# Kernel tuning notes

Measured on AMD Instinct MI355X. Metric: run time of the kernel, lower is better.

Reference implementation:

```python
import jax, jax.numpy as jnp
import numpy as np

DIM = 768
N_HEADS = 12
HEAD_DIM = DIM // N_HEADS
B, S = 2, 4096


def setup_inputs() -> dict:
    key = jax.random.key(0)
    k_x, k_wqkv, k_bqkv, k_wout, k_bout = jax.random.split(key, 5)
    scale_in = 1.0 / np.sqrt(DIM)
    return {
        "x": jax.random.normal(k_x, (B, S, DIM), dtype=jnp.float32),
        "Wqkv": jax.random.normal(k_wqkv, (DIM, 3 * DIM), dtype=jnp.float32) * scale_in,
        "bqkv": jax.random.normal(k_bqkv, (3 * DIM,), dtype=jnp.float32) * 0.02,
        "Wout": jax.random.normal(k_wout, (DIM, DIM), dtype=jnp.float32) * scale_in,
        "bout": jax.random.normal(k_bout, (DIM,), dtype=jnp.float32) * 0.02,
    }


def reference(x, Wqkv, bqkv, Wout, bout):
    b, s, d = x.shape
    qkv = (x @ Wqkv + bqkv).reshape(b, s, 3, N_HEADS, HEAD_DIM)
    qkv = jnp.transpose(qkv, (2, 0, 3, 1, 4))  # [3, B, H, S, hd]
    q, k, v = qkv[0], qkv[1], qkv[2]
    scale = HEAD_DIM ** -0.5
    attn = jnp.einsum('bhqd,bhkd->bhqk', q, k) * scale  # [B, H, S, S]
    causal_mask = jnp.triu(jnp.ones((s, s), dtype=bool), k=1)
    attn = jnp.where(causal_mask[None, None], -jnp.inf, attn)
    attn = jax.nn.softmax(attn, axis=-1)
    out = jnp.einsum('bhqk,bhkd->bhqd', attn, v)  # [B, H, S, hd]
    out = jnp.transpose(out, (0, 2, 1, 3)).reshape(b, s, d)
    return out @ Wout + bout
```

## Files before the change

### kernel.cpp

```cpp
#include <hip/hip_runtime.h>
#include <hip/hip_bf16.h>
#include <math.h>

#define DIM 768
#define NH 12
#define HD 64
#define BATCH 2
#define SEQ 4096
#define MTOT (BATCH * SEQ)

#define QSCALE 0.1803368801111244f

typedef unsigned short u16;
typedef __bf16 bf16x8 __attribute__((ext_vector_type(8)));
typedef float  f32x4  __attribute__((ext_vector_type(4)));
typedef float  f32x16 __attribute__((ext_vector_type(16)));
typedef unsigned short u16x4 __attribute__((ext_vector_type(4)));
typedef unsigned short u16x8 __attribute__((ext_vector_type(8)));
typedef unsigned u32x4 __attribute__((ext_vector_type(4)));

__device__ inline u16 f2bf(float f) {
    unsigned u = __builtin_bit_cast(unsigned, f);
    u += 0x7fffu + ((u >> 16) & 1u);
    return (u16)(u >> 16);
}

#if defined(__has_builtin) && __has_builtin(__builtin_amdgcn_cvt_pk_bf16_f32)
#define HAVE_PK_BF16 1
__device__ inline unsigned pk2bf(float a, float b) {
    auto v = __builtin_amdgcn_cvt_pk_bf16_f32(a, b);
    return __builtin_bit_cast(unsigned, v);
}
#else
#define HAVE_PK_BF16 0
__device__ inline unsigned pk2bf(float a, float b) {
    return (unsigned)f2bf(a) | ((unsigned)f2bf(b) << 16);
}
#endif

__device__ inline f32x4 mfma16(bf16x8 a, bf16x8 b, f32x4 c) {
    return __builtin_amdgcn_mfma_f32_16x16x32_bf16(a, b, c, 0, 0, 0);
}
__device__ inline f32x16 mfma32(bf16x8 a, bf16x8 b, f32x16 c) {
    return __builtin_amdgcn_mfma_f32_32x32x16_bf16(a, b, c, 0, 0, 0);
}

__device__ inline void gl2lds16(const u16* g, u16* l) {
    __builtin_amdgcn_global_load_lds(
        (const __attribute__((address_space(1))) void*)g,
        (__attribute__((address_space(3))) void*)l,
        16, 0, 0);
}

__global__ __launch_bounds__(256)
void cvt_bf16(const float* __restrict__ src, u16* __restrict__ dst, int n8)
{
    int i = blockIdx.x * 256 + threadIdx.x;
    if (i >= n8) return;
    float4 a = ((const float4*)src)[i * 2];
    float4 b = ((const float4*)src)[i * 2 + 1];
    u16x8 o;
    o[0] = f2bf(a.x); o[1] = f2bf(a.y); o[2] = f2bf(a.z); o[3] = f2bf(a.w);
    o[4] = f2bf(b.x); o[5] = f2bf(b.y); o[6] = f2bf(b.z); o[7] = f2bf(b.w);
    ((u16x8*)dst)[i] = o;
}

__global__ __launch_bounds__(256)
void transpose_to_bf16(const float* __restrict__ src, u16* __restrict__ dst,
                       int R, int C)
{
    __shared__ float tile[32][33];
    const int c0 = blockIdx.x * 32, r0 = blockIdx.y * 32;
    const int tx = threadIdx.x & 31, ty = threadIdx.x >> 5;
#pragma unroll
    for (int i = 0; i < 4; ++i) {
        int row = ty * 4 + i;
        tile[row][tx] = src[(size_t)(r0 + row) * C + c0 + tx];
    }
    __syncthreads();
#pragma unroll
    for (int i = 0; i < 4; ++i) {
        int crow = ty * 4 + i;
        dst[(size_t)(c0 + crow) * R + r0 + tx] = f2bf(tile[tx][crow]);
    }
}

__device__ inline void gemm_lds_mainloop(const u16* __restrict__ Ag,
                                         const u16* __restrict__ Bg,
                                         int m0, int n0, int w, int lane,
                                         u16 (*As)[64 * 64], u16 (*Bs)[64 * 64],
                                         f32x4 acc[4][4])
{
    const int quad = lane >> 4, lc = lane & 15;
    const int wm = (w & 1) * 64, wn = (w >> 1) * 64;
    const int drow = lane >> 3;
    const int dp   = lane & 7;

#pragma unroll
    for (int mi = 0; mi < 4; ++mi)
#pragma unroll
        for (int nj = 0; nj < 4; ++nj)
            acc[mi][nj] = f32x4{0.f, 0.f, 0.f, 0.f};

#pragma unroll
    for (int i = 0; i < 2; ++i) {
        const int r  = w * 16 + i * 8 + drow;
        const int g  = dp ^ (r & 7);
        const int tr = 2 * r + (g >> 2);
        const int kc = g & 3;
        gl2lds16(Ag + (size_t)(m0 + tr) * 768 + kc * 8, &As[0][(w * 16 + i * 8) * 64]);
        gl2lds16(Bg + (size_t)(n0 + tr) * 768 + kc * 8, &Bs[0][(w * 16 + i * 8) * 64]);
    }
    __syncthreads();

    for (int ks = 0; ks < 24; ++ks) {
        const int cur = ks & 1;

        if (ks < 23) {
            const int k0n = (ks + 1) * 32;
#pragma unroll
            for (int i = 0; i < 2; ++i) {
                const int r  = w * 16 + i * 8 + drow;
                const int g  = dp ^ (r & 7);
                const int tr = 2 * r + (g >> 2);
                const int kc = g & 3;
                gl2lds16(Ag + (size_t)(m0 + tr) * 768 + k0n + kc * 8,
                         &As[1 - cur][(w * 16 + i * 8) * 64]);
                gl2lds16(Bg + (size_t)(n0 + tr) * 768 + k0n + kc * 8,
                         &Bs[1 - cur][(w * 16 + i * 8) * 64]);
            }
        }

        bf16x8 af[4], bfr[4];
#pragma unroll
        for (int mi = 0; mi < 4; ++mi) {
            const int m = wm + mi * 16 + lc;
            const int r = m >> 1;
            const int p = (((m & 1) * 4 + quad)) ^ (r & 7);
            af[mi] = *(const bf16x8*)&As[cur][r * 64 + p * 8];
        }
#pragma unroll
        for (int nj = 0; nj < 4; ++nj) {
            const int n = wn + nj * 16 + lc;
            const int r = n >> 1;
            const int p = (((n & 1) * 4 + quad)) ^ (r & 7);
            bfr[nj] = *(const bf16x8*)&Bs[cur][r * 64 + p * 8];
        }

#pragma unroll
        for (int mi = 0; mi < 4; ++mi)
#pragma unroll
            for (int nj = 0; nj < 4; ++nj)
                acc[mi][nj] = mfma16(af[mi], bfr[nj], acc[mi][nj]);

        __syncthreads();
    }
}

__global__ __launch_bounds__(256)
void gemm_qkv_mfma(const u16* __restrict__ A, const u16* __restrict__ Bt,
                   const float* __restrict__ bias,
                   u16* __restrict__ Qb, u16* __restrict__ Kb, u16* __restrict__ Vt)
{
    __shared__ u16 As[2][64 * 64];
    __shared__ u16 Bs[2][64 * 64];
    const int m0 = blockIdx.x * 128;
    const int n0 = blockIdx.y * 128;
    const int t = threadIdx.x;
    const int w = t >> 6, lane = t & 63;
    const int quad = lane >> 4, lc = lane & 15;
    const int wm = (w & 1) * 64, wn = (w >> 1) * 64;

    f32x4 acc[4][4];
    gemm_lds_mainloop(A, Bt, m0, n0, w, lane, As, Bs, acc);

    const int b  = m0 >> 12;
    const int s0 = (m0 & 4095) + wm;
    const int nbase = n0 + wn;
    const int three = nbase / 768;
    const int rem   = nbase - three * 768;
    const int h     = rem >> 6;
    const int bh    = b * NH + h;

    if (three < 2) {
        u16* dst = (three == 0) ? Qb : Kb;
        const float qs = (three == 0) ? QSCALE : 1.0f;
#pragma unroll
        for (int nj = 0; nj < 4; ++nj) {
            const float bi = bias[nbase + nj * 16 + lc];
            const int d = nj * 16 + lc;
#pragma unroll
            for (int mi = 0; mi < 4; ++mi) {
                const int s = s0 + mi * 16 + quad * 4;
#pragma unroll
                for (int r = 0; r < 4; ++r)
                    dst[((size_t)bh * SEQ + s + r) * HD + d] = f2bf((acc[mi][nj][r] + bi) * qs);
            }
        }
    } else {
#pragma unroll
        for (int nj = 0; nj < 4; ++nj) {
            const float bi = bias[nbase + nj * 16 + lc];
            const int d = nj * 16 + lc;
            const size_t rowb = ((size_t)bh * HD + d) * SEQ;
#pragma unroll
            for (int mi = 0; mi < 4; ++mi) {
                const int s = s0 + mi * 16 + quad * 4;
                u16x4 wv;
#pragma unroll
                for (int r = 0; r < 4; ++r) wv[r] = f2bf(acc[mi][nj][r] + bi);
                *(u16x4*)&Vt[rowb + s] = wv;
            }
        }
    }
}

__global__ __launch_bounds__(256)
void gemm_out_mfma(const u16* __restrict__ A, const u16* __restrict__ Bt,
                   const float* __restrict__ bias, float* __restrict__ C)
{
    __shared__ u16 As[2][64 * 64];
    __shared__ u16 Bs[2][64 * 64];
    const int m0 = blockIdx.x * 128;
    const int n0 = blockIdx.y * 128;
    const int t = threadIdx.x;
    const int w = t >> 6, lane = t & 63;
    const int quad = lane >> 4, lc = lane & 15;
    const int wm = (w & 1) * 64, wn = (w >> 1) * 64;

    f32x4 acc[4][4];
    gemm_lds_mainloop(A, Bt, m0, n0, w, lane, As, Bs, acc);

#pragma unroll
    for (int nj = 0; nj < 4; ++nj) {
        const int col = n0 + wn + nj * 16 + lc;
        const float bi = bias[col];
#pragma unroll
        for (int mi = 0; mi < 4; ++mi) {
            const int row = m0 + wm + mi * 16 + quad * 4;
#pragma unroll
            for (int r = 0; r < 4; ++r)
                C[(size_t)(row + r) * 768 + col] = acc[mi][nj][r] + bi;
        }
    }
}

__global__ __launch_bounds__(256, 3)
void flash_attn(const u16* __restrict__ Qg, const u16* __restrict__ Kg,
                const u16* __restrict__ Vtg, u16* __restrict__ Og)
{
    const int bh   = blockIdx.x;
    const int pair = blockIdx.y;
    const int b    = bh / NH, h = bh % NH;
    const int t    = threadIdx.x;
    const int w    = t >> 6;
    const int wq   = w >> 1;
    const int wk   = w & 1;
    const int lane = t & 63;
    const int lc32 = lane & 31;
    const int hi   = lane >> 5;
    const int drow = lane >> 3;
    const int dp   = lane & 7;

    __shared__ u16 Ks[2][64 * 64];
    __shared__ u16 Vs[2][64 * 64];

    const u16* Qp = Qg  + (size_t)bh * SEQ * HD;
    const u16* Kp = Kg  + (size_t)bh * SEQ * HD;
    const u16* Vp = Vtg + (size_t)bh * HD * SEQ;
    float* Vscr = (float*)&Vs[0][0];
    float* Lx   = (float*)&Ks[0][0];

#pragma unroll 1
    for (int half = 0; half < 2; ++half) {
        const int qt    = half ? pair : (63 - pair);
        const int qrow0 = qt * 64 + wq * 32;

        bf16x8 qa[4];
#pragma unroll
        for (int ds = 0; ds < 4; ++ds)
            qa[ds] = *(const bf16x8*)
                &Qp[(size_t)(qrow0 + lc32) * HD + ds * 16 + hi * 8];

        f32x16 o2[2];
        o2[0] = f32x16{};
        o2[1] = f32x16{};
        float l_r = 0.f;

#pragma unroll
        for (int i = 0; i < 2; ++i) {
            const int r0  = w * 16 + i * 8;
            const int row = r0 + drow;
            const int gc  = dp ^ (row & 7);
            gl2lds16(Kp + (size_t)row * HD + gc * 8, &Ks[0][r0 * 64]);
            gl2lds16(Vp + (size_t)row * SEQ + gc * 8, &Vs[0][r0 * 64]);
        }
        __syncthreads();

        for (int tk = 0; tk <= qt; ++tk) {
            const int kb  = tk * 64;
            const int cur = tk & 1;

            if (tk < qt) {
                const int kbn = kb + 64;
#pragma unroll
                for (int i = 0; i < 2; ++i) {
                    const int r0  = w * 16 + i * 8;
                    const int row = r0 + drow;
                    const int gc  = dp ^ (row & 7);
                    gl2lds16(Kp + (size_t)(kbn + row) * HD + gc * 8,
                             &Ks[1 - cur][r0 * 64]);
                    gl2lds16(Vp + (size_t)row * SEQ + kbn + gc * 8,
                             &Vs[1 - cur][r0 * 64]);
                }
            }

            f32x16 sacc = {};
            {
                const int row = wk * 32 + lc32;
                const int sw  = row & 7;
#pragma unroll
                for (int ds = 0; ds < 4; ++ds) {
                    bf16x8 kf = *(const bf16x8*)
                        &Ks[cur][row * 64 + (((ds * 2 + hi) ^ sw) * 8)];
                    sacc = mfma32(kf, qa[ds], sacc);
                }
            }

            if (tk == qt) {
                const int q = qrow0 + lc32;
#pragma unroll
                for (int r = 0; r < 16; ++r) {
                    const int key = kb + wk * 32 + (r & 3) + 8 * (r >> 2) + 4 * hi;
                    if (key > q) sacc[r] = -1e30f;
                }
            }

            float pv[16];
#pragma unroll
            for (int r = 0; r < 16; ++r)
                pv[r] = __builtin_amdgcn_exp2f(sacc[r]);

            l_r += (((pv[0] + pv[1]) + (pv[2] + pv[3]))
                  + ((pv[4] + pv[5]) + (pv[6] + pv[7])))
                 + (((pv[8] + pv[9]) + (pv[10] + pv[11]))
                  + ((pv[12] + pv[13]) + (pv[14] + pv[15])));

            bf16x8 pa[2];
#pragma unroll
            for (int s = 0; s < 2; ++s) {
                unsigned w0 = pk2bf(pv[8 * s + 0], pv[8 * s + 1]);
                unsigned w1 = pk2bf(pv[8 * s + 2], pv[8 * s + 3]);
                unsigned w2 = pk2bf(pv[8 * s + 4], pv[8 * s + 5]);
                unsigned w3 = pk2bf(pv[8 * s + 6], pv[8 * s + 7]);
                asm("v_permlane32_swap_b32 %0, %1" : "+v"(w0), "+v"(w2));
                asm("v_permlane32_swap_b32 %0, %1" : "+v"(w1), "+v"(w3));
                u32x4 tw;
                tw[0] = w0; tw[1] = w1; tw[2] = w2; tw[3] = w3;
                pa[s] = __builtin_bit_cast(bf16x8, tw);
            }

#pragma unroll
            for (int dt = 0; dt < 2; ++dt) {
                const int row = dt * 32 + lc32;
                const int sw  = row & 7;
#pragma unroll
                for (int s = 0; s < 2; ++s) {
                    bf16x8 vf = *(const bf16x8*)
                        &Vs[cur][row * 64 + (((wk * 4 + s * 2 + hi) ^ sw) * 8)];
                    o2[dt] = mfma32(pa[s], vf, o2[dt]);
                }
            }

            __syncthreads();
        }

        const float lt = l_r + __shfl_xor(l_r, 32);

        if (wk == 1) {
#pragma unroll
            for (int dt = 0; dt < 2; ++dt)
#pragma unroll
                for (int r = 0; r < 16; ++r) {
                    const int ql = (r & 3) + 8 * (r >> 2) + 4 * hi;
                    Vscr[wq * 2048 + ql * 64 + dt * 32 + lc32] = o2[dt][r];
                }
            if (lane < 32) Lx[wq * 32 + lc32] = lt;
        }
        __syncthreads();
        if (wk == 0) {
            const float linv_q = 1.0f / (lt + Lx[wq * 32 + lc32]);
#pragma unroll
            for (int r = 0; r < 16; ++r) {
                const int ql   = (r & 3) + 8 * (r >> 2) + 4 * hi;
                const float li = __shfl(linv_q, ql);
                const int q = qrow0 + ql;
                const size_t base = ((size_t)(b * SEQ + q)) * DIM + h * HD + lc32;
#pragma unroll
                for (int dt = 0; dt < 2; ++dt) {
                    const float ov = o2[dt][r]
                        + Vscr[wq * 2048 + ql * 64 + dt * 32 + lc32];
                    Og[base + dt * 32] = f2bf(ov * li);
                }
            }
        }
        __syncthreads();
    }
}

extern "C" void kernel_launch(void* const* d_in, const int* in_sizes, int n_in,
                              void* d_out, int out_size, void* d_ws, size_t ws_size,
                              hipStream_t stream)
{
    const float* x    = (const float*)d_in[0];
    const float* Wqkv = (const float*)d_in[1];
    const float* bqkv = (const float*)d_in[2];
    const float* Wout = (const float*)d_in[3];
    const float* bout = (const float*)d_in[4];
    float* out = (float*)d_out;

    const size_t NX  = (size_t)MTOT * DIM;
    const size_t NWQ = (size_t)DIM * 3 * DIM;
    const size_t NWO = (size_t)DIM * DIM;
    u16* p   = (u16*)d_ws;
    u16* Xb  = p;              p += NX;
    u16* Wqt = p;              p += NWQ;
    u16* Wot = p;              p += NWO;
    u16* Qb  = p;              p += NX;
    u16* Kb  = p;              p += NX;
    u16* Vt  = p;              p += NX;
    u16* Ao  = p;

    cvt_bf16<<<(int)(NX / 8 + 255) / 256, 256, 0, stream>>>(x, Xb, (int)(NX / 8));
    transpose_to_bf16<<<dim3(2304 / 32, 768 / 32), 256, 0, stream>>>(Wqkv, Wqt, 768, 2304);
    transpose_to_bf16<<<dim3(768 / 32, 768 / 32), 256, 0, stream>>>(Wout, Wot, 768, 768);

    gemm_qkv_mfma<<<dim3(MTOT / 128, 2304 / 128), 256, 0, stream>>>(Xb, Wqt, bqkv, Qb, Kb, Vt);
    flash_attn<<<dim3(24, 32), 256, 0, stream>>>(Qb, Kb, Vt, Ao);
    gemm_out_mfma<<<dim3(MTOT / 128, 768 / 128), 256, 0, stream>>>(Ao, Wot, bout, out);
}
```

Baseline: 243.0 us.

## Triple-buffer K/V tiles with two-deep prefetch and explicit vmcnt waits

Changes the flash attention K/V staging from double to triple buffering in LDS, prefetching two tiles ahead. The blanket __syncthreads is replaced by partial s_waitcnt vmcnt counts plus s_barrier, so the tile in flight does not have to land before the next iteration starts. Q loads now come after the first prefetches so they overlap. This hides global load latency at the cost of 50% more LDS per block, which may reduce occupancy under launch_bounds(256,3), and it depends on the hand-written vmcnt counts being correct.

```diff
diff --git a/kernel.cpp b/kernel.cpp
--- a/kernel.cpp
+++ b/kernel.cpp
@@ -262,8 +262,8 @@
     const int drow = lane >> 3;
     const int dp   = lane & 7;
 
-    __shared__ u16 Ks[2][64 * 64];
-    __shared__ u16 Vs[2][64 * 64];
+    __shared__ u16 Ks[3][64 * 64];
+    __shared__ u16 Vs[3][64 * 64];
 
     const u16* Qp = Qg  + (size_t)bh * SEQ * HD;
     const u16* Kp = Kg  + (size_t)bh * SEQ * HD;
@@ -275,17 +275,6 @@
     for (int half = 0; half < 2; ++half) {
         const int qt    = half ? pair : (63 - pair);
         const int qrow0 = qt * 64 + wq * 32;
-
-        bf16x8 qa[4];
-#pragma unroll
-        for (int ds = 0; ds < 4; ++ds)
-            qa[ds] = *(const bf16x8*)
-                &Qp[(size_t)(qrow0 + lc32) * HD + ds * 16 + hi * 8];
-
-        f32x16 o2[2];
-        o2[0] = f32x16{};
-        o2[1] = f32x16{};
-        float l_r = 0.f;
 
 #pragma unroll
         for (int i = 0; i < 2; ++i) {
@@ -295,23 +284,48 @@
             gl2lds16(Kp + (size_t)row * HD + gc * 8, &Ks[0][r0 * 64]);
             gl2lds16(Vp + (size_t)row * SEQ + gc * 8, &Vs[0][r0 * 64]);
         }
-        __syncthreads();
-
+        if (qt >= 1) {
+#pragma unroll
+            for (int i = 0; i < 2; ++i) {
+                const int r0  = w * 16 + i * 8;
+                const int row = r0 + drow;
+                const int gc  = dp ^ (row & 7);
+                gl2lds16(Kp + (size_t)(64 + row) * HD + gc * 8, &Ks[1][r0 * 64]);
+                gl2lds16(Vp + (size_t)row * SEQ + 64 + gc * 8, &Vs[1][r0 * 64]);
+            }
+        }
+
+        bf16x8 qa[4];
+#pragma unroll
+        for (int ds = 0; ds < 4; ++ds)
+            qa[ds] = *(const bf16x8*)
+                &Qp[(size_t)(qrow0 + lc32) * HD + ds * 16 + hi * 8];
+
+        f32x16 o2[2];
+        o2[0] = f32x16{};
+        o2[1] = f32x16{};
+        float l_r = 0.f;
+
+        if (qt >= 1) { asm volatile("s_waitcnt vmcnt(8)" ::: "memory"); }
+        else         { asm volatile("s_waitcnt vmcnt(4)" ::: "memory"); }
+        __builtin_amdgcn_s_barrier();
+
+        int cur = 0;
         for (int tk = 0; tk <= qt; ++tk) {
-            const int kb  = tk * 64;
-            const int cur = tk & 1;
-
-            if (tk < qt) {
-                const int kbn = kb + 64;
+            const int kb = tk * 64;
+
+            if (tk + 2 <= qt) {
+                const int kb2 = kb + 128;
+                const int nb  = (cur >= 1) ? (cur - 1) : 2;
 #pragma unroll
                 for (int i = 0; i < 2; ++i) {
                     const int r0  = w * 16 + i * 8;
                     const int row = r0 + drow;
                     const int gc  = dp ^ (row & 7);
-                    gl2lds16(Kp + (size_t)(kbn + row) * HD + gc * 8,
-                             &Ks[1 - cur][r0 * 64]);
-                    gl2lds16(Vp + (size_t)row * SEQ + kbn + gc * 8,
-                             &Vs[1 - cur][r0 * 64]);
+                    gl2lds16(Kp + (size_t)(kb2 + row) * HD + gc * 8,
+                             &Ks[nb][r0 * 64]);
+                    gl2lds16(Vp + (size_t)row * SEQ + kb2 + gc * 8,
+                             &Vs[nb][r0 * 64]);
                 }
             }
 
@@ -372,7 +386,11 @@
                 }
             }
 
-            __syncthreads();
+            if (tk + 2 <= qt) { asm volatile("s_waitcnt vmcnt(4)" ::: "memory"); }
+            else              { asm volatile("s_waitcnt vmcnt(0)" ::: "memory"); }
+            __builtin_amdgcn_s_barrier();
+
+            cur = (cur == 2) ? 0 : cur + 1;
         }
 
         const float lt = l_r + __shfl_xor(l_r, 32);
```

Result: no change. 242.7 us (-0.1%).
